# Kernel tuning notes

Hardware: AMD Instinct MI355X
Metric: run time of the kernel (lower is better)

## Reference

```python
import jax, jax.numpy as jnp
import numpy as np
from jax import lax

B, N, C = 32, 512, 512   # N must be 8*8*8 (Convpass reshape)
H, DH = 8, 64            # heads, head_dim
ADIM = 8                 # adapter dim
MLP = 4096
EPS = 1e-5
SCALE = DH ** -0.5


def _ln(x, g, b):
    m = jnp.mean(x, axis=-1, keepdims=True)
    v = jnp.mean((x - m) ** 2, axis=-1, keepdims=True)
    return (x - m) * lax.rsqrt(v + EPS) * g + b


def _qgelu(x):
    return x * jax.nn.sigmoid(1.702 * x)


def _convpass(x, dw, db, cw, cb, uw, ub):
    # x: [B,N,C] -> down [B,N,ADIM]
    d = _qgelu(jnp.einsum('bnc,ca->bna', x, dw) + db)
    p = d.reshape(B, 8, 8, 8, ADIM).transpose(0, 4, 1, 2, 3)  # NCDHW
    p = lax.conv_general_dilated(
        p, cw, window_strides=(1, 1, 1), padding='SAME',
        dimension_numbers=('NCDHW', 'OIDHW', 'NCDHW')) + cb[None, :, None, None, None]
    p = p.transpose(0, 2, 3, 4, 1).reshape(B, N, ADIM)
    return jnp.einsum('bna,ac->bnc', _qgelu(p), uw) + ub


def _attn(x, qkv_w, proj_w, proj_b):
    qkv = jnp.einsum('bnc,ck->bnk', x, qkv_w)            # [B,N,3C]
    qkv = qkv.reshape(B, N, 3, H, DH)
    q, k, v = (qkv[:, :, i].transpose(0, 2, 1, 3) for i in range(3))  # [B,H,N,DH]
    a = jax.nn.softmax(jnp.einsum('bhnd,bhmd->bhnm', q, k) * SCALE, axis=-1)
    o = jnp.einsum('bhnm,bhmd->bhnd', a, v).transpose(0, 2, 1, 3).reshape(B, N, C)
    return jnp.einsum('bnc,ck->bnk', o, proj_w) + proj_b


def setup_inputs() -> dict:
    key = jax.random.key(0)
    ks = jax.random.split(key, 24)
    r = lambda i, shape, s=0.02: jax.random.normal(ks[i], shape, jnp.float32) * s
    inp = {
        'x': jax.random.normal(ks[0], (B, N, C), jnp.float32),
        'pos': jax.random.normal(ks[1], (B, N, C), jnp.float32),
        'ln1_g': jnp.ones((C,), jnp.float32), 'ln1_b': jnp.zeros((C,), jnp.float32),
        'qkv_w': r(2, (C, 3 * C)),
        'proj_w': r(3, (C, C)), 'proj_b': jnp.zeros((C,), jnp.float32),
        'cp1_down_w': r(4, (C, ADIM)), 'cp1_down_b': jnp.zeros((ADIM,), jnp.float32),
        'cp1_conv_w': r(5, (ADIM, ADIM, 3, 3, 3), 0.1), 'cp1_conv_b': jnp.zeros((ADIM,), jnp.float32),
        'cp1_up_w': r(6, (ADIM, C)), 'cp1_up_b': jnp.zeros((C,), jnp.float32),
        'ln2_g': jnp.ones((C,), jnp.float32), 'ln2_b': jnp.zeros((C,), jnp.float32),
        'ff_w1': r(7, (C, MLP)), 'ff_b1': jnp.zeros((MLP,), jnp.float32),
        'ff_w2': r(8, (MLP, C)), 'ff_b2': jnp.zeros((C,), jnp.float32),
        'cp2_down_w': r(9, (C, ADIM)), 'cp2_down_b': jnp.zeros((ADIM,), jnp.float32),
        'cp2_conv_w': r(10, (ADIM, ADIM, 3, 3, 3), 0.1), 'cp2_conv_b': jnp.zeros((ADIM,), jnp.float32),
        'cp2_up_w': r(11, (ADIM, C)), 'cp2_up_b': jnp.zeros((C,), jnp.float32),
    }
    return inp


def reference(x, pos, ln1_g, ln1_b, qkv_w, proj_w, proj_b,
              cp1_down_w, cp1_down_b, cp1_conv_w, cp1_conv_b, cp1_up_w, cp1_up_b,
              ln2_g, ln2_b, ff_w1, ff_b1, ff_w2, ff_b2,
              cp2_down_w, cp2_down_b, cp2_conv_w, cp2_conv_b, cp2_up_w, cp2_up_b):
    x = x + pos
    # attention stage: Residual(PreNormDrop(LN, SelfAttn, Convpass)), dropout=identity (eval)
    h = _ln(x, ln1_g, ln1_b)
    x = x + _attn(h, qkv_w, proj_w, proj_b) + _convpass(h, cp1_down_w, cp1_down_b, cp1_conv_w, cp1_conv_b, cp1_up_w, cp1_up_b)
    # FFN stage: Residual(PreNorm(LN, FFN, Convpass))
    h = _ln(x, ln2_g, ln2_b)
    ffn = jnp.einsum('bnm,mc->bnc', jax.nn.gelu(jnp.einsum('bnc,cm->bnm', h, ff_w1) + ff_b1, approximate=False), ff_w2) + ff_b2
    x = x + ffn + _convpass(h, cp2_down_w, cp2_down_b, cp2_conv_w, cp2_conv_b, cp2_up_w, cp2_up_b)
    return x
```

## Files before the change

### kernel.cpp

```cpp
#include <hip/hip_runtime.h>
#include <math.h>

typedef __bf16 bf16_t;
typedef __bf16 bf16x8 __attribute__((ext_vector_type(8)));
typedef __bf16 bf16x4 __attribute__((ext_vector_type(4)));
typedef float f32x4 __attribute__((ext_vector_type(4)));

constexpr int kB   = 32;
constexpr int kN   = 512;
constexpr int kC   = 512;
constexpr int kH   = 8;
constexpr int kAD  = 8;
constexpr int kMLP = 4096;
constexpr int kBN  = kB * kN;
constexpr float kEPS   = 1e-5f;
constexpr float kSCALE = 0.125f;

__device__ __forceinline__ float qgelu_f(float x) {
    return x / (1.f + __expf(-1.702f * x));
}
__device__ __forceinline__ float gelu_f(float x) {
    float u = 1.5957691216f * x * (1.f + 0.044715f * x * x);
    float e = __expf(u);
    float th = 1.f - 2.f / (e + 1.f);
    return 0.5f * x * (1.f + th);
}

__device__ __forceinline__ unsigned pk2(float a, float b) {
    union { bf16_t h[2]; unsigned u; } z;
    z.h[0] = (bf16_t)a; z.h[1] = (bf16_t)b;
    return z.u;
}

__device__ __forceinline__ void gld_lds16(const void* g, void* l) {
    typedef const __attribute__((address_space(1))) unsigned int* gp_t;
    typedef __attribute__((address_space(3))) unsigned int* lp_t;
    __builtin_amdgcn_global_load_lds((gp_t)(unsigned long long)g,
                                     (lp_t)(unsigned)(unsigned long long)l,
                                     16, 0, 0);
}

__global__ __launch_bounds__(256) void k_addln(
    const float* __restrict__ x, const float* __restrict__ pos,
    const float* __restrict__ g, const float* __restrict__ be,
    float* __restrict__ xout, bf16_t* __restrict__ hout,
    const float* __restrict__ cpv, const float* __restrict__ uwp,
    const float* __restrict__ ubp)
{
    int row = blockIdx.x, tid = threadIdx.x;
    size_t base = (size_t)row * kC;
    __shared__ float s8[8];
    if (cpv) {
        if (tid < 8) s8[tid] = cpv[(size_t)row * 8 + tid];
        __syncthreads();
    }
    float v0 = x[base + tid], v1 = x[base + tid + 256];
    if (pos) { v0 += pos[base + tid]; v1 += pos[base + tid + 256]; }
    if (cpv) {
        float u0 = ubp[tid], u1 = ubp[tid + 256];
        #pragma unroll
        for (int a = 0; a < 8; a++) {
            u0 += s8[a] * uwp[a * kC + tid];
            u1 += s8[a] * uwp[a * kC + tid + 256];
        }
        v0 += u0; v1 += u1;
    }
    if (xout) { xout[base + tid] = v0; xout[base + tid + 256] = v1; }
    float s = v0 + v1, q = v0 * v0 + v1 * v1;
    #pragma unroll
    for (int o = 32; o > 0; o >>= 1) {
        s += __shfl_down(s, o);
        q += __shfl_down(q, o);
    }
    __shared__ float ss[4], sq[4], mrs[2];
    int wv = tid >> 6, ln = tid & 63;
    if (!ln) { ss[wv] = s; sq[wv] = q; }
    __syncthreads();
    if (!tid) {
        float ts = ss[0] + ss[1] + ss[2] + ss[3];
        float tq = sq[0] + sq[1] + sq[2] + sq[3];
        float m = ts * (1.f / kC);
        float var = tq * (1.f / kC) - m * m;
        mrs[0] = m; mrs[1] = rsqrtf(var + kEPS);
    }
    __syncthreads();
    float m = mrs[0], r = mrs[1];
    hout[base + tid]       = (bf16_t)((v0 - m) * r * g[tid] + be[tid]);
    hout[base + tid + 256] = (bf16_t)((v1 - m) * r * g[tid + 256] + be[tid + 256]);
}

__global__ __launch_bounds__(256) void k_transpose_all(
    const float* __restrict__ qkvw, const float* __restrict__ projw,
    const float* __restrict__ fw1,  const float* __restrict__ fw2,
    bf16_t* __restrict__ qkvT, bf16_t* __restrict__ projT,
    bf16_t* __restrict__ fw1T, bf16_t* __restrict__ fw2T)
{
    int id = blockIdx.x;
    const float* w; bf16_t* wt; int K, N, bx, by;
    if (id < 768)       { w = qkvw; wt = qkvT; K = 512;  N = 1536; bx = id % 48;  by = id / 48; }
    else if (id < 1024) { id -= 768;  w = projw; wt = projT; K = 512;  N = 512;  bx = id % 16;  by = id / 16; }
    else if (id < 3072) { id -= 1024; w = fw1;   wt = fw1T;  K = 512;  N = 4096; bx = id % 128; by = id / 128; }
    else                { id -= 3072; w = fw2;   wt = fw2T;  K = 4096; N = 512;  bx = id % 16;  by = id / 16; }
    __shared__ float t[32][33];
    int n0 = bx * 32, k0 = by * 32;
    int tx = threadIdx.x & 31, ty = threadIdx.x >> 5;
    #pragma unroll
    for (int j = 0; j < 32; j += 8)
        t[ty + j][tx] = w[(size_t)(k0 + ty + j) * N + n0 + tx];
    __syncthreads();
    #pragma unroll
    for (int j = 0; j < 32; j += 8)
        wt[(size_t)(n0 + ty + j) * K + k0 + tx] = (bf16_t)t[tx][ty + j];
}

template <int ACT, bool HASB, bool HASR, int OMODE, int K, int LDA, int LDB, int NC>
__global__ __launch_bounds__(256) void k_gemm(
    const bf16_t* __restrict__ A, const bf16_t* __restrict__ Bt,
    const float* __restrict__ bias, const float* __restrict__ res,
    void* __restrict__ outv)
{
    __shared__ bf16_t As[2][128 * 32];
    __shared__ bf16_t Bs[2][128 * 32];
    int tid = threadIdx.x;
    int nbx = gridDim.x;
    int flat = blockIdx.y * nbx + blockIdx.x;
    int chunk = (nbx * gridDim.y) >> 3;
    int flat2 = (flat & 7) * chunk + (flat >> 3);
    int col0 = (flat2 % nbx) * 128, row0 = (flat2 / nbx) * 128;
    int w = tid >> 6, l = tid & 63;
    int rw0 = (w & 1) * 64, cw0 = (w >> 1) * 64;
    int lr = tid >> 2;
    int lc = (((tid & 3) ^ ((tid >> 3) & 3)) * 8);

    f32x4 acc[4][4];
    #pragma unroll
    for (int i = 0; i < 4; i++)
        #pragma unroll
        for (int j = 0; j < 4; j++)
            acc[i][j] = (f32x4){0.f, 0.f, 0.f, 0.f};

    const bf16_t* Ag  = A  + (size_t)(row0 + lr) * LDA + lc;
    const bf16_t* Ag2 = A  + (size_t)(row0 + 64 + lr) * LDA + lc;
    const bf16_t* Bg  = Bt + (size_t)(col0 + lr) * LDB + lc;
    const bf16_t* Bg2 = Bt + (size_t)(col0 + 64 + lr) * LDB + lc;

    int am = rw0 + (l & 15);
    int bn = cw0 + (l & 15);
    int kq = (l >> 4) * 8;
    int kqA = kq ^ (((am >> 1) & 3) << 3);
    int kqB = kq ^ (((bn >> 1) & 3) << 3);

    for (int k0 = 0; k0 < K; k0 += 64) {
        gld_lds16(Ag + k0, &As[0][tid * 8]);
        gld_lds16(Ag2 + k0, &As[0][2048 + tid * 8]);
        gld_lds16(Bg + k0, &Bs[0][tid * 8]);
        gld_lds16(Bg2 + k0, &Bs[0][2048 + tid * 8]);
        gld_lds16(Ag + k0 + 32, &As[1][tid * 8]);
        gld_lds16(Ag2 + k0 + 32, &As[1][2048 + tid * 8]);
        gld_lds16(Bg + k0 + 32, &Bs[1][tid * 8]);
        gld_lds16(Bg2 + k0 + 32, &Bs[1][2048 + tid * 8]);
        __syncthreads();
        #pragma unroll
        for (int ks = 0; ks < 2; ks++) {
            bf16x8 af[4], bfr[4];
            #pragma unroll
            for (int mt = 0; mt < 4; mt++)
                af[mt] = *(const bf16x8*)&As[ks][(am + mt * 16) * 32 + kqA];
            #pragma unroll
            for (int nt = 0; nt < 4; nt++)
                bfr[nt] = *(const bf16x8*)&Bs[ks][(bn + nt * 16) * 32 + kqB];
            #pragma unroll
            for (int mt = 0; mt < 4; mt++)
                #pragma unroll
                for (int nt = 0; nt < 4; nt++)
                    acc[mt][nt] = __builtin_amdgcn_mfma_f32_16x16x32_bf16(
                        af[mt], bfr[nt], acc[mt][nt], 0, 0, 0);
        }
        __syncthreads();
    }

    #pragma unroll
    for (int mt = 0; mt < 4; mt++) {
        int rowb = row0 + rw0 + mt * 16 + (l >> 4) * 4;
        #pragma unroll
        for (int nt = 0; nt < 4; nt++) {
            int col = col0 + cw0 + nt * 16 + (l & 15);
            float bv = HASB ? bias[col] : 0.f;
            if (OMODE == 2) {
                int which = col >> 9, hd = (col >> 6) & 7, d = col & 63;
                size_t hb = ((size_t)((rowb >> 9) * 8 + hd) * 3 + which) << 15;
                int n0 = rowb & 511;
                if (which == 2) {
                    bf16x4 pk;
                    #pragma unroll
                    for (int p = 0; p < 4; p++) pk[p] = (bf16_t)acc[mt][nt][p];
                    *(bf16x4*)((bf16_t*)outv + hb + (size_t)d * 512 + n0) = pk;
                } else {
                    #pragma unroll
                    for (int p = 0; p < 4; p++)
                        ((bf16_t*)outv)[hb + (size_t)(n0 + p) * 64 + d] =
                            (bf16_t)acc[mt][nt][p];
                }
            } else {
                #pragma unroll
                for (int p = 0; p < 4; p++) {
                    float v = acc[mt][nt][p] + bv;
                    if (ACT == 1) v = qgelu_f(v);
                    if (ACT == 2) v = gelu_f(v);
                    int r = rowb + p;
                    if (OMODE == 0) {
                        if (HASR) v += res[(size_t)r * NC + col];
                        ((float*)outv)[(size_t)r * NC + col] = v;
                    } else {
                        ((bf16_t*)outv)[(size_t)r * NC + col] = (bf16_t)v;
                    }
                }
            }
        }
    }
}

__global__ __launch_bounds__(256) void k_attn(
    const bf16_t* __restrict__ qkvb, bf16_t* __restrict__ obuf)
{
    __shared__ __align__(16) unsigned Ps[4][16 * 36];
    int bid = blockIdx.x;
    bid = (bid & 7) * 128 + (bid >> 3);
    int qb = bid & 3, h = (bid >> 2) & 7, b = bid >> 5;
    int t = threadIdx.x, w = t >> 6, l = t & 63;
    const bf16_t* qp  = qkvb + (((size_t)(b * 8 + h) * 3) << 15);
    const bf16_t* kp  = qp + (1 << 15);
    const bf16_t* vtp = qp + (2 << 15);
    int q0 = qb * 128 + w * 32;
    int l15 = l & 15, g = l >> 4, lq = g * 8;
    unsigned* psw = &Ps[w][0];

    bf16x8 aq[2][2];
    #pragma unroll
    for (int mt = 0; mt < 2; mt++)
        #pragma unroll
        for (int kh = 0; kh < 2; kh++) {
            bf16x8 qv = *(const bf16x8*)(qp + (size_t)(q0 + mt * 16 + l15) * 64
                                         + kh * 32 + lq);
            #pragma unroll
            for (int e = 0; e < 8; e++) qv[e] = (bf16_t)((float)qv[e] * kSCALE);
            aq[mt][kh] = qv;
        }

    f32x4 o[2][4];
    float l_part[2];
    #pragma unroll
    for (int mt = 0; mt < 2; mt++) {
        l_part[mt] = 0.f;
        #pragma unroll
        for (int dt = 0; dt < 4; dt++) o[mt][dt] = (f32x4){0.f, 0.f, 0.f, 0.f};
    }

    for (int kt = 0; kt < 8; kt++) {
        bf16x8 kf[4][2], vf[4][2];
        #pragma unroll
        for (int nt = 0; nt < 4; nt++)
            #pragma unroll
            for (int kh = 0; kh < 2; kh++)
                kf[nt][kh] = *(const bf16x8*)(kp
                    + (size_t)(kt * 64 + nt * 16 + l15) * 64 + kh * 32 + lq);
        #pragma unroll
        for (int dt = 0; dt < 4; dt++)
            #pragma unroll
            for (int kh = 0; kh < 2; kh++)
                vf[dt][kh] = *(const bf16x8*)(vtp
                    + (size_t)(dt * 16 + l15) * 512 + kt * 64 + kh * 32 + lq);

        #pragma unroll
        for (int mt = 0; mt < 2; mt++) {
            f32x4 sc[4];
            #pragma unroll
            for (int nt = 0; nt < 4; nt++) sc[nt] = (f32x4){0.f, 0.f, 0.f, 0.f};
            #pragma unroll
            for (int nt = 0; nt < 4; nt++)
                #pragma unroll
                for (int kh = 0; kh < 2; kh++)
                    sc[nt] = __builtin_amdgcn_mfma_f32_16x16x32_bf16(
                        kf[nt][kh], aq[mt][kh], sc[nt], 0, 0, 0);
            #pragma unroll
            for (int nt = 0; nt < 4; nt++)
                #pragma unroll
                for (int p = 0; p < 4; p++)
                    sc[nt][p] = __expf(sc[nt][p] - 8.0f);
            #pragma unroll
            for (int nt = 0; nt < 4; nt++) {
                uint2 dw;
                dw.x = pk2(sc[nt][0], sc[nt][1]);
                dw.y = pk2(sc[nt][2], sc[nt][3]);
                *(uint2*)&psw[l15 * 36 + nt * 8 + g * 2] = dw;
            }
            float r0 = (sc[0][0] + sc[0][1]) + (sc[0][2] + sc[0][3]);
            float r1 = (sc[1][0] + sc[1][1]) + (sc[1][2] + sc[1][3]);
            float r2 = (sc[2][0] + sc[2][1]) + (sc[2][2] + sc[2][3]);
            float r3 = (sc[3][0] + sc[3][1]) + (sc[3][2] + sc[3][3]);
            l_part[mt] += (r0 + r1) + (r2 + r3);
            asm volatile("" ::: "memory");
            bf16x8 pf0 = *(const bf16x8*)&psw[l15 * 36 + g * 4];
            bf16x8 pf1 = *(const bf16x8*)&psw[l15 * 36 + 16 + g * 4];
            #pragma unroll
            for (int dt = 0; dt < 4; dt++) {
                o[mt][dt] = __builtin_amdgcn_mfma_f32_16x16x32_bf16(
                    vf[dt][0], pf0, o[mt][dt], 0, 0, 0);
                o[mt][dt] = __builtin_amdgcn_mfma_f32_16x16x32_bf16(
                    vf[dt][1], pf1, o[mt][dt], 0, 0, 0);
            }
            asm volatile("" ::: "memory");
        }
    }
    #pragma unroll
    for (int mt = 0; mt < 2; mt++) {
        float lr = l_part[mt];
        lr += __shfl_xor(lr, 16);
        lr += __shfl_xor(lr, 32);
        float inv = 1.f / lr;
        size_t rbase = ((size_t)b * 512 + q0 + mt * 16 + l15) * 512 + h * 64;
        #pragma unroll
        for (int dt = 0; dt < 4; dt++) {
            bf16x4 pk;
            #pragma unroll
            for (int p = 0; p < 4; p++) pk[p] = (bf16_t)(o[mt][dt][p] * inv);
            *(bf16x4*)&obuf[rbase + dt * 16 + g * 4] = pk;
        }
    }
}

__global__ __launch_bounds__(256) void k_down(
    const bf16_t* __restrict__ h, const float* __restrict__ dw,
    const float* __restrict__ db, float* __restrict__ outp)
{
    __shared__ float sdw[kC * kAD];
    int t = threadIdx.x;
    for (int i = t; i < kC * kAD; i += 256) sdw[i] = dw[i];
    __syncthreads();
    int gt = blockIdx.x * 256 + t;
    int row = gt >> 3, a = gt & 7;
    const bf16x8* hr = (const bf16x8*)(h + (size_t)row * kC);
    float acc = 0.f;
    for (int k8 = 0; k8 < kC / 8; k8++) {
        bf16x8 hv = hr[k8];
        #pragma unroll
        for (int e = 0; e < 8; e++)
            acc += (float)hv[e] * sdw[(k8 * 8 + e) * kAD + a];
    }
    outp[gt] = qgelu_f(acc + db[a]);
}

__global__ __launch_bounds__(512) void k_conv(
    const float* __restrict__ inp, const float* __restrict__ cw,
    const float* __restrict__ cb, float* __restrict__ outp)
{
    __shared__ float si[512 * 9];
    __shared__ float sw[8 * 8 * 27];
    int b = blockIdx.x, t = threadIdx.x;
    for (int i = t; i < 512 * 8; i += 512) {
        int n = i >> 3, a = i & 7;
        si[n * 9 + a] = inp[(size_t)b * 4096 + i];
    }
    for (int i = t; i < 1728; i += 512) sw[i] = cw[i];
    __syncthreads();
    int z = t >> 6, y = (t >> 3) & 7, xx = t & 7;
    float acc[8];
    #pragma unroll
    for (int ao = 0; ao < 8; ao++) acc[ao] = cb[ao];
    for (int dz = -1; dz <= 1; dz++) {
        int zz = z + dz; if ((unsigned)zz > 7u) continue;
        for (int dy = -1; dy <= 1; dy++) {
            int yy = y + dy; if ((unsigned)yy > 7u) continue;
            for (int dx = -1; dx <= 1; dx++) {
                int xn = xx + dx; if ((unsigned)xn > 7u) continue;
                int nn = zz * 64 + yy * 8 + xn;
                int wo = ((dz + 1) * 3 + (dy + 1)) * 3 + (dx + 1);
                #pragma unroll
                for (int ai = 0; ai < 8; ai++) {
                    float iv = si[nn * 9 + ai];
                    #pragma unroll
                    for (int ao = 0; ao < 8; ao++)
                        acc[ao] += iv * sw[(ao * 8 + ai) * 27 + wo];
                }
            }
        }
    }
    #pragma unroll
    for (int ao = 0; ao < 8; ao++)
        outp[(size_t)b * 4096 + t * 8 + ao] = qgelu_f(acc[ao]);
}

__global__ __launch_bounds__(256) void k_up(
    const float* __restrict__ pa, const float* __restrict__ uw,
    const float* __restrict__ ub, float* __restrict__ xbuf)
{
    __shared__ float s[8];
    int row = blockIdx.x, t = threadIdx.x;
    if (t < 8) s[t] = pa[(size_t)row * kAD + t];
    __syncthreads();
    #pragma unroll
    for (int rep = 0; rep < 2; rep++) {
        int c = t + rep * 256;
        float acc = ub[c];
        #pragma unroll
        for (int a = 0; a < 8; a++) acc += s[a] * uw[a * kC + c];
        xbuf[(size_t)row * kC + c] += acc;
    }
}

extern "C" void kernel_launch(void* const* d_in, const int* in_sizes, int n_in,
                              void* d_out, int out_size, void* d_ws, size_t ws_size,
                              hipStream_t stream)
{
    const float* x     = (const float*)d_in[0];
    const float* pos   = (const float*)d_in[1];
    const float* ln1g  = (const float*)d_in[2];
    const float* ln1b  = (const float*)d_in[3];
    const float* qkvw  = (const float*)d_in[4];
    const float* projw = (const float*)d_in[5];
    const float* projb = (const float*)d_in[6];
    const float* dw1   = (const float*)d_in[7];
    const float* db1   = (const float*)d_in[8];
    const float* cw1   = (const float*)d_in[9];
    const float* cb1   = (const float*)d_in[10];
    const float* uw1   = (const float*)d_in[11];
    const float* ub1   = (const float*)d_in[12];
    const float* ln2g  = (const float*)d_in[13];
    const float* ln2b  = (const float*)d_in[14];
    const float* fw1   = (const float*)d_in[15];
    const float* fb1   = (const float*)d_in[16];
    const float* fw2   = (const float*)d_in[17];
    const float* fb2   = (const float*)d_in[18];
    const float* dw2   = (const float*)d_in[19];
    const float* db2   = (const float*)d_in[20];
    const float* cw2   = (const float*)d_in[21];
    const float* cb2   = (const float*)d_in[22];
    const float* uw2   = (const float*)d_in[23];
    const float* ub2   = (const float*)d_in[24];
    float* out = (float*)d_out;

    char* wsb = (char*)d_ws;
    float*  xbuf = (float*)wsb;
    bf16_t* hb   = (bf16_t*)(wsb + 33554432);
    bf16_t* obuf = (bf16_t*)(wsb + 50331648);
    bf16_t* qkvb = (bf16_t*)(wsb + 67108864);
    bf16_t* midb = (bf16_t*)(wsb + 50331648);
    bf16_t* qkvT = (bf16_t*)(wsb + 117440512);
    bf16_t* projT= (bf16_t*)(wsb + 119013376);
    bf16_t* fw1T = (bf16_t*)(wsb + 119537664);
    bf16_t* fw2T = (bf16_t*)(wsb + 123731968);
    float*  cpa  = (float*)(wsb + 127926272);
    float*  cpb  = (float*)(wsb + 128450560);

    k_transpose_all<<<5120, 256, 0, stream>>>(
        qkvw, projw, fw1, fw2, qkvT, projT, fw1T, fw2T);

    k_addln<<<kBN, 256, 0, stream>>>(x, pos, ln1g, ln1b, xbuf, hb,
                                     nullptr, nullptr, nullptr);

    k_gemm<0, false, false, 2, 512, 512, 512, 1536>
        <<<dim3(12, 128), 256, 0, stream>>>(hb, qkvT, nullptr, nullptr, qkvb);
    k_attn<<<kB * kH * 4, 256, 0, stream>>>(qkvb, obuf);
    k_gemm<0, true, true, 0, 512, 512, 512, 512>
        <<<dim3(4, 128), 256, 0, stream>>>(obuf, projT, projb, xbuf, xbuf);

    k_down<<<kBN * kAD / 256, 256, 0, stream>>>(hb, dw1, db1, cpa);
    k_conv<<<kB, 512, 0, stream>>>(cpa, cw1, cb1, cpb);

    k_addln<<<kBN, 256, 0, stream>>>(xbuf, nullptr, ln2g, ln2b, xbuf, hb,
                                     cpb, uw1, ub1);

    k_down<<<kBN * kAD / 256, 256, 0, stream>>>(hb, dw2, db2, cpa);
    k_conv<<<kB, 512, 0, stream>>>(cpa, cw2, cb2, cpb);
    k_up<<<kBN, 256, 0, stream>>>(cpb, uw2, ub2, xbuf);

    k_gemm<2, true, false, 1, 512, 512, 512, 2048>
        <<<dim3(16, 128), 256, 0, stream>>>(hb, fw1T, fb1, nullptr, midb);
    k_gemm<0, false, true, 0, 2048, 2048, 4096, 512>
        <<<dim3(4, 128), 256, 0, stream>>>(midb, fw2T, nullptr, xbuf, xbuf);
    k_gemm<2, true, false, 1, 512, 512, 512, 2048>
        <<<dim3(16, 128), 256, 0, stream>>>(hb, fw1T + (size_t)2048 * 512,
                                            fb1 + 2048, nullptr, midb);
    k_gemm<0, true, true, 0, 2048, 2048, 4096, 512>
        <<<dim3(4, 128), 256, 0, stream>>>(midb, fw2T + 2048, fb2, xbuf, out);
}
```

Before: 633.9 us.

## Double-buffer GEMM LDS tiles to overlap global loads with MFMA

Splits the GEMM shared-memory tiles into two ping-pong buffers, so the next 64-wide K slab is loaded asynchronously into LDS while MFMAs run on the current one. This hides the global-load latency that previously stalled each iteration at the barrier. It doubles LDS use per block to 64KB, which may reduce occupancy. It also rewrites gelu and qgelu to use a hardware reciprocal and FMAs instead of divisions.

```diff
diff --git a/kernel.cpp b/kernel.cpp
--- a/kernel.cpp
+++ b/kernel.cpp
@@ -17,13 +17,15 @@
 constexpr float kSCALE = 0.125f;
 
 __device__ __forceinline__ float qgelu_f(float x) {
-    return x / (1.f + __expf(-1.702f * x));
+    float e = __expf(-1.702f * x);
+    return x * __builtin_amdgcn_rcpf(1.f + e);
 }
 __device__ __forceinline__ float gelu_f(float x) {
-    float u = 1.5957691216f * x * (1.f + 0.044715f * x * x);
-    float e = __expf(u);
-    float th = 1.f - 2.f / (e + 1.f);
-    return 0.5f * x * (1.f + th);
+    float t = x * x;
+    float p = __builtin_fmaf(0.044715f, t, 1.f);
+    float e = __expf(1.5957691216f * x * p);
+    float r = __builtin_amdgcn_rcpf(1.f + e);
+    return __builtin_fmaf(-x, r, x);
 }
 
 __device__ __forceinline__ unsigned pk2(float a, float b) {
@@ -119,8 +121,8 @@
     const float* __restrict__ bias, const float* __restrict__ res,
     void* __restrict__ outv)
 {
-    __shared__ bf16_t As[2][128 * 32];
-    __shared__ bf16_t Bs[2][128 * 32];
+    __shared__ bf16_t As[2][2][128 * 32];
+    __shared__ bf16_t Bs[2][2][128 * 32];
     int tid = threadIdx.x;
     int nbx = gridDim.x;
     int flat = blockIdx.y * nbx + blockIdx.x;
@@ -150,34 +152,47 @@
     int kqA = kq ^ (((am >> 1) & 3) << 3);
     int kqB = kq ^ (((bn >> 1) & 3) << 3);
 
-    for (int k0 = 0; k0 < K; k0 += 64) {
-        gld_lds16(Ag + k0, &As[0][tid * 8]);
-        gld_lds16(Ag2 + k0, &As[0][2048 + tid * 8]);
-        gld_lds16(Bg + k0, &Bs[0][tid * 8]);
-        gld_lds16(Bg2 + k0, &Bs[0][2048 + tid * 8]);
-        gld_lds16(Ag + k0 + 32, &As[1][tid * 8]);
-        gld_lds16(Ag2 + k0 + 32, &As[1][2048 + tid * 8]);
-        gld_lds16(Bg + k0 + 32, &Bs[1][tid * 8]);
-        gld_lds16(Bg2 + k0 + 32, &Bs[1][2048 + tid * 8]);
+#define STAGEG(P, K0) do {                                                  \
+    gld_lds16(Ag + (K0),       &As[P][0][tid * 8]);                         \
+    gld_lds16(Ag2 + (K0),      &As[P][0][2048 + tid * 8]);                  \
+    gld_lds16(Bg + (K0),       &Bs[P][0][tid * 8]);                         \
+    gld_lds16(Bg2 + (K0),      &Bs[P][0][2048 + tid * 8]);                  \
+    gld_lds16(Ag + (K0) + 32,  &As[P][1][tid * 8]);                         \
+    gld_lds16(Ag2 + (K0) + 32, &As[P][1][2048 + tid * 8]);                  \
+    gld_lds16(Bg + (K0) + 32,  &Bs[P][1][tid * 8]);                         \
+    gld_lds16(Bg2 + (K0) + 32, &Bs[P][1][2048 + tid * 8]);                  \
+  } while (0)
+
+#define COMPUTEG(P) do {                                                    \
+    _Pragma("unroll")                                                       \
+    for (int ks = 0; ks < 2; ks++) {                                        \
+        bf16x8 af[4], bfr[4];                                               \
+        _Pragma("unroll")                                                   \
+        for (int mt = 0; mt < 4; mt++)                                      \
+            af[mt] = *(const bf16x8*)&As[P][ks][(am + mt * 16) * 32 + kqA]; \
+        _Pragma("unroll")                                                   \
+        for (int nt = 0; nt < 4; nt++)                                      \
+            bfr[nt] = *(const bf16x8*)&Bs[P][ks][(bn + nt * 16) * 32 + kqB];\
+        _Pragma("unroll")                                                   \
+        for (int mt = 0; mt < 4; mt++)                                      \
+            _Pragma("unroll")                                               \
+            for (int nt = 0; nt < 4; nt++)                                  \
+                acc[mt][nt] = __builtin_amdgcn_mfma_f32_16x16x32_bf16(      \
+                    af[mt], bfr[nt], acc[mt][nt], 0, 0, 0);                 \
+    }                                                                       \
+  } while (0)
+
+    STAGEG(0, 0);
+    for (int k0 = 0; k0 < K; k0 += 128) {
         __syncthreads();
-        #pragma unroll
-        for (int ks = 0; ks < 2; ks++) {
-            bf16x8 af[4], bfr[4];
-            #pragma unroll
-            for (int mt = 0; mt < 4; mt++)
-                af[mt] = *(const bf16x8*)&As[ks][(am + mt * 16) * 32 + kqA];
-            #pragma unroll
-            for (int nt = 0; nt < 4; nt++)
-                bfr[nt] = *(const bf16x8*)&Bs[ks][(bn + nt * 16) * 32 + kqB];
-            #pragma unroll
-            for (int mt = 0; mt < 4; mt++)
-                #pragma unroll
-                for (int nt = 0; nt < 4; nt++)
-                    acc[mt][nt] = __builtin_amdgcn_mfma_f32_16x16x32_bf16(
-                        af[mt], bfr[nt], acc[mt][nt], 0, 0, 0);
-        }
+        STAGEG(1, k0 + 64);
+        COMPUTEG(0);
         __syncthreads();
-    }
+        if (k0 + 128 < K) STAGEG(0, k0 + 128);
+        COMPUTEG(1);
+    }
+#undef STAGEG
+#undef COMPUTEG
 
     #pragma unroll
     for (int mt = 0; mt < 4; mt++) {
```

Result: no change. 623.8 us (-1.6%).
